# Kernel tuning notes

Measured on AMD Instinct MI355X. Metric: run time of the kernel, lower is better.

Reference implementation:

```python
import jax, jax.numpy as jnp
import numpy as np

N, NFEAT, NHID, NREL, NCLASS, NHEADS = 4096, 512, 64, 64, 16, 8
ALPHA = 0.2   # LeakyReLU negative slope
NEG = -9e15   # pyGAT mask value


def _gat_layer(x, rel, mask, adj_ad, W, a1, a2, concat):
    # x: [N, Fin], rel: [nrel, Fin], mask: [N, N] bool, adj_ad: [N, nrel]
    xr = x + adj_ad @ rel                 # relation-augmented node features
    h = xr @ W                            # [N, Fout]
    f1 = h @ a1                           # [N]  (a^T[Wh_i||Wh_j] = f1_i + f2_j)
    f2 = h @ a2                           # [N]
    e = jax.nn.leaky_relu(f1[:, None] + f2[None, :], ALPHA)  # [N, N]
    att = jax.nn.softmax(jnp.where(mask, e, NEG), axis=1)
    out = att @ h                         # [N, Fout]
    return jax.nn.elu(out) if concat else out


def setup_inputs() -> dict:
    key = jax.random.key(0)
    ks = jax.random.split(key, 12)
    x = jax.random.normal(ks[0], (N, NFEAT), jnp.float32)
    rel = jax.random.normal(ks[1], (NREL, NFEAT), jnp.float32)
    rel_dict = jax.random.randint(ks[2], (N,), 0, NREL, jnp.int32)
    adj = (jax.random.uniform(ks[3], (N, N)) < 0.01).astype(jnp.float32)
    adj = jnp.maximum(adj, jnp.eye(N, dtype=jnp.float32))  # self loops
    adj_ad = jax.random.uniform(ks[4], (N, NREL), jnp.float32)
    adj_ad = adj_ad / adj_ad.sum(axis=1, keepdims=True)
    s_in = 1.0 / np.sqrt(NFEAT)
    s_hid = 1.0 / np.sqrt(NHID)
    s_cat = 1.0 / np.sqrt(NHID * NHEADS)
    W_heads = jax.random.normal(ks[5], (NHEADS, NFEAT, NHID), jnp.float32) * s_in
    a1_heads = jax.random.normal(ks[6], (NHEADS, NHID), jnp.float32) * s_hid
    a2_heads = jax.random.normal(ks[7], (NHEADS, NHID), jnp.float32) * s_hid
    W_out = jax.random.normal(ks[8], (NHID * NHEADS, NFEAT), jnp.float32) * s_cat
    a1_out = jax.random.normal(ks[9], (NFEAT,), jnp.float32) * s_in
    a2_out = jax.random.normal(ks[10], (NFEAT,), jnp.float32) * s_in
    lin_W = jax.random.normal(ks[11], (NFEAT, NCLASS), jnp.float32) * s_in
    lin_b = jnp.zeros((NCLASS,), jnp.float32)
    return {"x": x, "rel": rel, "rel_dict": rel_dict, "adj": adj, "adj_ad": adj_ad,
            "W_heads": W_heads, "a1_heads": a1_heads, "a2_heads": a2_heads,
            "W_out": W_out, "a1_out": a1_out, "a2_out": a2_out,
            "lin_W": lin_W, "lin_b": lin_b}


def reference(x, rel, rel_dict, adj, adj_ad, W_heads, a1_heads, a2_heads,
              W_out, a1_out, a2_out, lin_W, lin_b):
    # dropout is identity at inference (training=False); rel_dict is only used
    # by the repo to build adj/adj_ad, so it is a non-math constant here.
    mask = adj > 0
    # multi-head GAT layer, heads fused via vmap then concatenated on feature dim
    heads = jax.vmap(lambda W, a1, a2: _gat_layer(x, rel, mask, adj_ad, W, a1, a2, True))(
        W_heads, a1_heads, a2_heads)                      # [H, N, NHID]
    hcat = jnp.moveaxis(heads, 0, 1).reshape(N, NHEADS * NHID)  # [N, H*NHID]
    h2 = _gat_layer(hcat, rel, mask, adj_ad, W_out, a1_out, a2_out, False)  # [N, NFEAT]
    logits = jax.nn.elu(h2 @ lin_W + lin_b)               # [N, NCLASS]
    return jax.nn.log_softmax(logits, axis=1)
```

## Files before the change

### kernel.cpp

```cpp
#include <hip/hip_runtime.h>

#define NN      4096
#define FEAT    512
#define KDIM    576
#define NHID    64
#define NHEADS  8
#define NCLS    16
#define MAXDEG  128
#define ALPHA   0.2f

typedef __bf16 bf16_t;
typedef __bf16 bf16x8_t __attribute__((ext_vector_type(8)));
typedef float  f32x4_t  __attribute__((ext_vector_type(4)));
typedef unsigned short us8_t __attribute__((ext_vector_type(8)));

__device__ inline unsigned short f2bf(float f) {
    unsigned int u = __float_as_uint(f);
    u += 0x7fffu + ((u >> 16) & 1u);
    return (unsigned short)(u >> 16);
}
__device__ inline float bfu2f(unsigned short b) {
    return __uint_as_float(((unsigned int)b) << 16);
}
__device__ inline void gload16(const void* g, void* s) {
    __builtin_amdgcn_global_load_lds(
        (const __attribute__((address_space(1))) void*)g,
        (__attribute__((address_space(3))) void*)s, 16, 0, 0);
}

#define PREP_REL0   0
#define PREP_TR0    256
#define PREP_Z0     384
#define PREP_CAST0  392
#define PREP_CSR0   2440
#define PREP_NBLK   3464

__global__ __launch_bounds__(256) void prep_kernel(
    const float* __restrict__ adj, int* __restrict__ deg, int* __restrict__ cols,
    const float* __restrict__ adj_ad, const float* __restrict__ rel,
    const float* __restrict__ x, bf16_t* __restrict__ Abf,
    bf16_t* __restrict__ Abf2,
    const float* __restrict__ Wh, const float* __restrict__ Wo,
    unsigned short* __restrict__ WcT, unsigned short* __restrict__ WoT,
    float* __restrict__ f1o, float* __restrict__ f2o) {
    int b = blockIdx.x;
    int t = threadIdx.x;
    __shared__ float smem[64 * 65];
    if (b < PREP_TR0) {
        int r  = b & 63;
        int nh = (b >> 6) & 1;
        int n  = nh * 256 + t;
        smem[t]       = rel[r * FEAT + t];
        smem[t + 256] = rel[r * FEAT + 256 + t];
        __syncthreads();
        float acc[8] = {};
        if (b < 128) {
            int h = n >> 6, f = n & 63;
            const float* p = Wh + (size_t)h * 32768 + f;
            for (int k0 = 0; k0 < 512; k0 += 8)
                #pragma unroll
                for (int u = 0; u < 8; ++u)
                    acc[u] += smem[k0 + u] * p[(size_t)(k0 + u) * 64];
            float s = ((acc[0] + acc[1]) + (acc[2] + acc[3]))
                    + ((acc[4] + acc[5]) + (acc[6] + acc[7]));
            WcT[(size_t)n * KDIM + 512 + r] = f2bf(s);
        } else {
            const float* p = Wo + n;
            for (int k0 = 0; k0 < 512; k0 += 8)
                #pragma unroll
                for (int u = 0; u < 8; ++u)
                    acc[u] += smem[k0 + u] * p[(size_t)(k0 + u) * 512];
            float s = ((acc[0] + acc[1]) + (acc[2] + acc[3]))
                    + ((acc[4] + acc[5]) + (acc[6] + acc[7]));
            WoT[(size_t)n * KDIM + 512 + r] = f2bf(s);
        }
    } else if (b < PREP_Z0) {
        int tb = b - PREP_TR0;
        if (tb < 64) {
            int h = tb >> 3, k0 = (tb & 7) * 64;
            const float* src = Wh + (size_t)h * 32768 + (size_t)k0 * 64;
            #pragma unroll
            for (int i2 = 0; i2 < 16; ++i2) {
                int li = t + i2 * 256;
                float v = src[li];
                smem[(li & 63) * 65 + (li >> 6)] = v;
            }
            __syncthreads();
            #pragma unroll
            for (int i2 = 0; i2 < 16; ++i2) {
                int li = t + i2 * 256;
                int f = li >> 6, r = li & 63;
                WcT[(size_t)(h * 64 + f) * KDIM + k0 + r] = f2bf(smem[f * 65 + r]);
            }
        } else {
            int wb = tb - 64;
            int n0 = (wb & 7) * 64, k0 = (wb >> 3) * 64;
            #pragma unroll
            for (int i2 = 0; i2 < 16; ++i2) {
                int li = t + i2 * 256;
                int r = li >> 6, f = li & 63;
                float v = Wo[(size_t)(k0 + r) * 512 + n0 + f];
                smem[f * 65 + r] = v;
            }
            __syncthreads();
            #pragma unroll
            for (int i2 = 0; i2 < 16; ++i2) {
                int li = t + i2 * 256;
                int f = li >> 6, r = li & 63;
                WoT[(size_t)(n0 + f) * KDIM + k0 + r] = f2bf(smem[f * 65 + r]);
            }
        }
    } else if (b < PREP_CAST0) {
        int g = (b - PREP_Z0) * 256 + t;
        if (g < 1024) ((float4*)f1o)[g] = make_float4(0.f, 0.f, 0.f, 0.f);
        else ((float4*)f2o)[g - 1024] = make_float4(0.f, 0.f, 0.f, 0.f);
    } else if (b < PREP_CSR0) {
        int half = t >> 7;
        int tt = t & 127;
        size_t i = (size_t)(b - PREP_CAST0) * 2 + half;
        float4 xv = ((const float4*)(x + i * FEAT))[tt];
        ushort4 o;
        o.x = f2bf(xv.x); o.y = f2bf(xv.y);
        o.z = f2bf(xv.z); o.w = f2bf(xv.w);
        *(ushort4*)(Abf + i * KDIM + 4 * tt) = o;
        if (tt < 16) {
            float4 av = ((const float4*)(adj_ad + i * 64))[tt];
            ushort4 o2;
            o2.x = f2bf(av.x); o2.y = f2bf(av.y);
            o2.z = f2bf(av.z); o2.w = f2bf(av.w);
            *(ushort4*)(Abf  + i * KDIM + 512 + 4 * tt) = o2;
            *(ushort4*)(Abf2 + i * KDIM + 512 + 4 * tt) = o2;
        }
    } else {
        int l = t & 63;
        int i = (b - PREP_CSR0) * 4 + (t >> 6);
        const float4* row4 = (const float4*)(adj + (size_t)i * NN);
        float4 v[16];
        #pragma unroll
        for (int c2 = 0; c2 < 16; ++c2) v[c2] = row4[l + c2 * 64];
        unsigned long long mask = 0;
        #pragma unroll
        for (int c2 = 0; c2 < 16; ++c2) {
            unsigned m4 = (unsigned)(v[c2].x > 0.0f)
                        | ((unsigned)(v[c2].y > 0.0f) << 1)
                        | ((unsigned)(v[c2].z > 0.0f) << 2)
                        | ((unsigned)(v[c2].w > 0.0f) << 3);
            mask |= (unsigned long long)m4 << (4 * c2);
        }
        int c = __popcll(mask);
        int pre = c;
        #pragma unroll
        for (int off = 1; off < 64; off <<= 1) {
            int n = __shfl_up(pre, off);
            if (l >= off) pre += n;
        }
        int base = pre - c;
        if (l == 63) deg[i] = pre > MAXDEG ? MAXDEG : pre;
        int* colrow = cols + i * MAXDEG;
        int idx = base;
        while (mask) {
            int bit = (int)__ffsll(mask) - 1;
            mask &= mask - 1;
            int j = 4 * l + ((bit >> 2) << 8) + (bit & 3);
            if (idx < MAXDEG) colrow[idx] = j;
            ++idx;
        }
    }
}

__global__ __launch_bounds__(256) void gemm_bf16_dot_kernel(
    const bf16_t* __restrict__ A, const bf16_t* __restrict__ Bt,
    unsigned short* __restrict__ Cbf,
    const float* __restrict__ a1, const float* __restrict__ a2,
    float* __restrict__ f1, float* __restrict__ f2, int layer2) {
    __shared__ __align__(16) bf16_t As[128][64];
    __shared__ __align__(16) bf16_t Bs[128][64];
    const int bm = blockIdx.x * 128;
    const int bn = blockIdx.y * 128;
    const int by = blockIdx.y;
    const int t  = threadIdx.x;
    const int l  = t & 63;
    const int w  = t >> 6;
    const int wr = w >> 1;
    const int wc = w & 1;
    const int c16 = l & 15;
    const int q8  = (l >> 4) * 8;
    const int r4  = (l >> 4) * 4;

    const bf16_t* Abase = A  + (size_t)bm * KDIM;
    const bf16_t* Bbase = Bt + (size_t)bn * KDIM;

    f32x4_t acc[4][4] = {};
    for (int k0 = 0; k0 < KDIM; k0 += 64) {
        #pragma unroll
        for (int c = 0; c < 4; ++c) {
            int cb = c * 256 + w * 64;
            int li = cb + l;
            gload16(Abase + (size_t)(li >> 3) * KDIM + k0 + (li & 7) * 8,
                    (char*)&As[0][0] + cb * 16);
        }
        #pragma unroll
        for (int c = 0; c < 4; ++c) {
            int cb = c * 256 + w * 64;
            int li = cb + l;
            gload16(Bbase + (size_t)(li >> 3) * KDIM + k0 + (li & 7) * 8,
                    (char*)&Bs[0][0] + cb * 16);
        }
        __syncthreads();
        #pragma unroll
        for (int kk = 0; kk < 64; kk += 32) {
            bf16x8_t af[4], bfr[4];
            #pragma unroll
            for (int mi = 0; mi < 4; ++mi)
                af[mi] = *(const bf16x8_t*)&As[wr * 64 + mi * 16 + c16][kk + q8];
            #pragma unroll
            for (int ni = 0; ni < 4; ++ni)
                bfr[ni] = *(const bf16x8_t*)&Bs[wc * 64 + ni * 16 + c16][kk + q8];
            #pragma unroll
            for (int mi = 0; mi < 4; ++mi)
                #pragma unroll
                for (int ni = 0; ni < 4; ++ni)
                    acc[mi][ni] = __builtin_amdgcn_mfma_f32_16x16x32_bf16(
                        af[mi], bfr[ni], acc[mi][ni], 0, 0, 0);
        }
        __syncthreads();
    }
    #pragma unroll
    for (int mi = 0; mi < 4; ++mi)
        #pragma unroll
        for (int ni = 0; ni < 4; ++ni)
            #pragma unroll
            for (int r = 0; r < 4; ++r)
                Cbf[(size_t)(bm + wr * 64 + mi * 16 + r4 + r) * FEAT
                    + bn + wc * 64 + ni * 16 + c16] = f2bf(acc[mi][ni][r]);

    float a1v[4], a2v[4];
    #pragma unroll
    for (int ni = 0; ni < 4; ++ni) {
        a1v[ni] = a1[bn + wc * 64 + ni * 16 + c16];
        a2v[ni] = a2[bn + wc * 64 + ni * 16 + c16];
    }
    float p1[4][4] = {}, p2[4][4] = {};
    #pragma unroll
    for (int mi = 0; mi < 4; ++mi)
        #pragma unroll
        for (int ni = 0; ni < 4; ++ni)
            #pragma unroll
            for (int r = 0; r < 4; ++r) {
                p1[mi][r] += acc[mi][ni][r] * a1v[ni];
                p2[mi][r] += acc[mi][ni][r] * a2v[ni];
            }
    #pragma unroll
    for (int off = 1; off <= 8; off <<= 1)
        #pragma unroll
        for (int mi = 0; mi < 4; ++mi)
            #pragma unroll
            for (int r = 0; r < 4; ++r) {
                p1[mi][r] += __shfl_xor(p1[mi][r], off);
                p2[mi][r] += __shfl_xor(p2[mi][r], off);
            }
    if (c16 == 0) {
        #pragma unroll
        for (int mi = 0; mi < 4; ++mi)
            #pragma unroll
            for (int r = 0; r < 4; ++r) {
                int row = bm + wr * 64 + mi * 16 + r4 + r;
                if (layer2) {
                    atomicAdd(&f1[row], p1[mi][r]);
                    atomicAdd(&f2[row], p2[mi][r]);
                } else {
                    f1[(by * 2 + wc) * NN + row] = p1[mi][r];
                    f2[(by * 2 + wc) * NN + row] = p2[mi][r];
                }
            }
    }
}

__global__ __launch_bounds__(512) void att1_kernel(
    const bf16_t* __restrict__ Hbf, const float* __restrict__ f1,
    const float* __restrict__ f2, const int* __restrict__ deg,
    const int* __restrict__ cols, bf16_t* __restrict__ outbf) {
    int i = blockIdx.x;
    int tid = threadIdx.x;
    int h = tid >> 6;
    int l = tid & 63;
    __shared__ int jl[MAXDEG];
    __shared__ float se[NHEADS][MAXDEG];
    __shared__ float part[NHEADS][FEAT];
    __shared__ float sinv[NHEADS];
    __shared__ int sdeg;
    if (tid == 0) sdeg = deg[i];
    __syncthreads();
    int d = sdeg;
    int dpad = (d + 63) & ~63;
    for (int k = tid; k < dpad; k += 512)
        jl[k] = (k < d) ? cols[i * MAXDEG + k] : i;
    __syncthreads();
    float fi = f1[h * NN + i];
    float lmax = -1e30f;
    for (int k = l; k < d; k += 64) {
        float e = fi + f2[h * NN + jl[k]];
        e = e > 0.0f ? e : ALPHA * e;
        se[h][k] = e;
        lmax = fmaxf(lmax, e);
    }
    for (int off = 32; off; off >>= 1) lmax = fmaxf(lmax, __shfl_down(lmax, off));
    float m = __shfl(lmax, 0);
    float ls = 0.0f;
    for (int k = l; k < d; k += 64) {
        float p = __expf(se[h][k] - m);
        se[h][k] = p;
        ls += p;
    }
    for (int k = d + l; k < dpad; k += 64) se[h][k] = 0.0f;
    for (int off = 32; off; off >>= 1) ls += __shfl_down(ls, off);
    if (l == 0) sinv[h] = 1.0f / ls;
    __syncthreads();
    const int myhead = l >> 3;
    float acc[8] = {};
    for (int k0 = 0; k0 < dpad; k0 += 64) {
        float pw[8];
        const bf16_t* rp[8];
        #pragma unroll
        for (int j = 0; j < 8; ++j) {
            int k = k0 + j * 8 + h;
            pw[j] = se[myhead][k];
            rp[j] = Hbf + (size_t)jl[k] * FEAT + l * 8;
        }
        #pragma unroll
        for (int j = 0; j < 8; ++j) {
            us8_t v = *(const us8_t*)rp[j];
            float p = pw[j];
            #pragma unroll
            for (int q = 0; q < 8; ++q) acc[q] += p * bfu2f(v[q]);
        }
    }
    *(float4*)&part[h][l * 8]     = make_float4(acc[0], acc[1], acc[2], acc[3]);
    *(float4*)&part[h][l * 8 + 4] = make_float4(acc[4], acc[5], acc[6], acc[7]);
    __syncthreads();
    {
        float sum = 0.0f;
        #pragma unroll
        for (int w2 = 0; w2 < NHEADS; ++w2) sum += part[w2][tid];
        float o = sum * sinv[tid >> 6];
        o = o > 0.0f ? o : __expf(o) - 1.0f;
        ((unsigned short*)outbf)[(size_t)i * KDIM + tid] = f2bf(o);
    }
}

__global__ __launch_bounds__(256) void att2_final_kernel(
    const bf16_t* __restrict__ Hbf, const float* __restrict__ f1,
    const float* __restrict__ f2, const int* __restrict__ deg,
    const int* __restrict__ cols, const float* __restrict__ linW,
    const float* __restrict__ linb, float* __restrict__ out) {
    int i = blockIdx.x;
    int t = threadIdx.x;
    __shared__ int jl[MAXDEG];
    __shared__ float sp[MAXDEG];
    __shared__ float red[4];
    __shared__ float part[3][FEAT];
    __shared__ float hrow[FEAT];
    __shared__ float clsred[16][NCLS];
    __shared__ float sl[NCLS];
    __shared__ int sdeg;
    if (t == 0) sdeg = deg[i];
    __syncthreads();
    int d = sdeg;
    int dpad = (d + 31) & ~31;
    if (t < dpad) jl[t] = (t < d) ? cols[i * MAXDEG + t] : i;
    __syncthreads();
    float e = 0.0f, lmax = -1e30f;
    if (t < d) {
        e = f1[i] + f2[jl[t]];
        e = e > 0.0f ? e : ALPHA * e;
        lmax = e;
    }
    for (int off = 32; off; off >>= 1) lmax = fmaxf(lmax, __shfl_down(lmax, off));
    if ((t & 63) == 0) red[t >> 6] = lmax;
    __syncthreads();
    float m = fmaxf(fmaxf(red[0], red[1]), fmaxf(red[2], red[3]));
    float p = 0.0f;
    if (t < d) p = __expf(e - m);
    if (t < dpad) sp[t] = p;
    float ls = p;
    for (int off = 32; off; off >>= 1) ls += __shfl_down(ls, off);
    __syncthreads();
    if ((t & 63) == 0) red[t >> 6] = ls;
    __syncthreads();
    float s = red[0] + red[1] + red[2] + red[3];
    float inv = 1.0f / s;
    const int slot = t >> 6;
    const int cg   = t & 63;
    float acc[8] = {};
    for (int k0 = 0; k0 < dpad; k0 += 32) {
        float pw[8];
        const bf16_t* rp[8];
        #pragma unroll
        for (int j = 0; j < 8; ++j) {
            int k = k0 + j * 4 + slot;
            pw[j] = sp[k];
            rp[j] = Hbf + (size_t)jl[k] * FEAT + cg * 8;
        }
        #pragma unroll
        for (int j = 0; j < 8; ++j) {
            us8_t v = *(const us8_t*)rp[j];
            float pk = pw[j];
            #pragma unroll
            for (int q = 0; q < 8; ++q) acc[q] += pk * bfu2f(v[q]);
        }
    }
    if (slot > 0) {
        float* dst = &part[slot - 1][cg * 8];
        *(float4*)(dst)     = make_float4(acc[0], acc[1], acc[2], acc[3]);
        *(float4*)(dst + 4) = make_float4(acc[4], acc[5], acc[6], acc[7]);
    }
    __syncthreads();
    if (slot == 0) {
        #pragma unroll
        for (int sl2 = 0; sl2 < 3; ++sl2)
            #pragma unroll
            for (int j = 0; j < 8; ++j) acc[j] += part[sl2][cg * 8 + j];
        float* dst = &hrow[cg * 8];
        *(float4*)(dst)     = make_float4(acc[0] * inv, acc[1] * inv, acc[2] * inv, acc[3] * inv);
        *(float4*)(dst + 4) = make_float4(acc[4] * inv, acc[5] * inv, acc[6] * inv, acc[7] * inv);
    }
    __syncthreads();
    {
        int c = t & 15;
        int seg = t >> 4;
        float partial = 0.0f;
        int f0 = seg * 32;
        #pragma unroll 8
        for (int f = f0; f < f0 + 32; ++f) partial += hrow[f] * linW[f * NCLS + c];
        clsred[seg][c] = partial;
    }
    __syncthreads();
    if (t < NCLS) {
        float logit = linb[t];
        #pragma unroll
        for (int seg = 0; seg < 16; ++seg) logit += clsred[seg][t];
        logit = logit > 0.0f ? logit : __expf(logit) - 1.0f;
        sl[t] = logit;
    }
    __syncthreads();
    if (t < NCLS) {
        float mm = sl[0];
        #pragma unroll
        for (int c = 1; c < NCLS; ++c) mm = fmaxf(mm, sl[c]);
        float ssum = 0.0f;
        #pragma unroll
        for (int c = 0; c < NCLS; ++c) ssum += __expf(sl[c] - mm);
        out[i * NCLS + t] = sl[t] - mm - logf(ssum);
    }
}

extern "C" void kernel_launch(void* const* d_in, const int* in_sizes, int n_in,
                              void* d_out, int out_size, void* d_ws, size_t ws_size,
                              hipStream_t stream) {
    const float* x        = (const float*)d_in[0];
    const float* rel      = (const float*)d_in[1];
    const float* adj      = (const float*)d_in[3];
    const float* adj_ad   = (const float*)d_in[4];
    const float* W_heads  = (const float*)d_in[5];
    const float* a1_heads = (const float*)d_in[6];
    const float* a2_heads = (const float*)d_in[7];
    const float* W_out    = (const float*)d_in[8];
    const float* a1_out   = (const float*)d_in[9];
    const float* a2_out   = (const float*)d_in[10];
    const float* lin_W    = (const float*)d_in[11];
    const float* lin_b    = (const float*)d_in[12];
    float* out = (float*)d_out;

    char* ws = (char*)d_ws;
    bf16_t* Abf  = (bf16_t*)(ws);
    bf16_t* Abf2 = (bf16_t*)(ws + (5u  << 20));
    bf16_t* Hbf1 = (bf16_t*)(ws + (10u << 20));
    bf16_t* Hbf2 = (bf16_t*)(ws + (14u << 20));
    bf16_t* WcT  = (bf16_t*)(ws + (18u << 20));
    bf16_t* WoT  = (bf16_t*)(ws + (19u << 20));
    float*  f1   = (float*) (ws + (20u << 20));
    float*  f2   = (float*) (ws + (20u << 20) + (128u << 10));
    float*  f1o  = (float*) (ws + (20u << 20) + (256u << 10));
    float*  f2o  = (float*) (ws + (20u << 20) + (272u << 10));
    int*    deg  = (int*)   (ws + (20u << 20) + (288u << 10));
    int*    cols = (int*)   (ws + (21u << 20));

    prep_kernel<<<PREP_NBLK, 256, 0, stream>>>(
        adj, deg, cols, adj_ad, rel, x, Abf, Abf2, W_heads, W_out,
        (unsigned short*)WcT, (unsigned short*)WoT, f1o, f2o);
    gemm_bf16_dot_kernel<<<dim3(32, 4), 256, 0, stream>>>(
        Abf, WcT, (unsigned short*)Hbf1, a1_heads, a2_heads, f1, f2, 0);
    att1_kernel<<<NN, 512, 0, stream>>>(Hbf1, f1, f2, deg, cols, Abf2);
    gemm_bf16_dot_kernel<<<dim3(32, 4), 256, 0, stream>>>(
        Abf2, WoT, (unsigned short*)Hbf2, a1_out, a2_out, f1o, f2o, 1);
    att2_final_kernel<<<NN, 256, 0, stream>>>(Hbf2, f1o, f2o, deg, cols, lin_W, lin_b, out);
}
```

Baseline: 207.4 us.

## Shrink GEMM tiles to 64x64 with XOR-swizzled LDS and trim attention padding

Halves the GEMM block tile from 128x128 to 64x64. This launches 512 workgroups instead of 128, so the grid can fill the GPU's compute units. An XOR swizzle is added to the LDS layout to avoid bank conflicts. Layer-1 f1/f2 partial dot products are now reduced per head with atomics into a zeroed buffer, and the prep kernel zeroes the whole contiguous f1/f2/f1o/f2o region. The attention kernels pad neighbor lists to smaller multiples, 32 and 16, to cut wasted gathers. In exchange, the smaller tiles reuse each loaded tile less and the change adds atomic traffic.

```diff
diff --git a/kernel.cpp b/kernel.cpp
--- a/kernel.cpp
+++ b/kernel.cpp
@@ -31,9 +31,9 @@
 #define PREP_REL0   0
 #define PREP_TR0    256
 #define PREP_Z0     384
-#define PREP_CAST0  392
-#define PREP_CSR0   2440
-#define PREP_NBLK   3464
+#define PREP_CAST0  456
+#define PREP_CSR0   2504
+#define PREP_NBLK   3528
 
 __global__ __launch_bounds__(256) void prep_kernel(
     const float* __restrict__ adj, int* __restrict__ deg, int* __restrict__ cols,
@@ -42,7 +42,7 @@
     bf16_t* __restrict__ Abf2,
     const float* __restrict__ Wh, const float* __restrict__ Wo,
     unsigned short* __restrict__ WcT, unsigned short* __restrict__ WoT,
-    float* __restrict__ f1o, float* __restrict__ f2o) {
+    float* __restrict__ fzero) {
     int b = blockIdx.x;
     int t = threadIdx.x;
     __shared__ float smem[64 * 65];
@@ -112,8 +112,7 @@
         }
     } else if (b < PREP_CAST0) {
         int g = (b - PREP_Z0) * 256 + t;
-        if (g < 1024) ((float4*)f1o)[g] = make_float4(0.f, 0.f, 0.f, 0.f);
-        else ((float4*)f2o)[g - 1024] = make_float4(0.f, 0.f, 0.f, 0.f);
+        ((float4*)fzero)[g] = make_float4(0.f, 0.f, 0.f, 0.f);
     } else if (b < PREP_CSR0) {
         int half = t >> 7;
         int tt = t & 127;
@@ -173,10 +172,10 @@
     unsigned short* __restrict__ Cbf,
     const float* __restrict__ a1, const float* __restrict__ a2,
     float* __restrict__ f1, float* __restrict__ f2, int layer2) {
-    __shared__ __align__(16) bf16_t As[128][64];
-    __shared__ __align__(16) bf16_t Bs[128][64];
-    const int bm = blockIdx.x * 128;
-    const int bn = blockIdx.y * 128;
+    __shared__ __align__(16) bf16_t As[64][64];
+    __shared__ __align__(16) bf16_t Bs[64][64];
+    const int bm = blockIdx.x * 64;
+    const int bn = blockIdx.y * 64;
     const int by = blockIdx.y;
     const int t  = threadIdx.x;
     const int l  = t & 63;
@@ -190,61 +189,70 @@
     const bf16_t* Abase = A  + (size_t)bm * KDIM;
     const bf16_t* Bbase = Bt + (size_t)bn * KDIM;
 
-    f32x4_t acc[4][4] = {};
+    f32x4_t acc[2][2] = {};
     for (int k0 = 0; k0 < KDIM; k0 += 64) {
         #pragma unroll
-        for (int c = 0; c < 4; ++c) {
+        for (int c = 0; c < 2; ++c) {
             int cb = c * 256 + w * 64;
             int li = cb + l;
-            gload16(Abase + (size_t)(li >> 3) * KDIM + k0 + (li & 7) * 8,
+            int r = li >> 3, pc = li & 7;
+            int lc = pc ^ (r & 7);
+            gload16(Abase + (size_t)r * KDIM + k0 + lc * 8,
                     (char*)&As[0][0] + cb * 16);
         }
         #pragma unroll
-        for (int c = 0; c < 4; ++c) {
+        for (int c = 0; c < 2; ++c) {
             int cb = c * 256 + w * 64;
             int li = cb + l;
-            gload16(Bbase + (size_t)(li >> 3) * KDIM + k0 + (li & 7) * 8,
+            int r = li >> 3, pc = li & 7;
+            int lc = pc ^ (r & 7);
+            gload16(Bbase + (size_t)r * KDIM + k0 + lc * 8,
                     (char*)&Bs[0][0] + cb * 16);
         }
         __syncthreads();
         #pragma unroll
         for (int kk = 0; kk < 64; kk += 32) {
-            bf16x8_t af[4], bfr[4];
-            #pragma unroll
-            for (int mi = 0; mi < 4; ++mi)
-                af[mi] = *(const bf16x8_t*)&As[wr * 64 + mi * 16 + c16][kk + q8];
-            #pragma unroll
-            for (int ni = 0; ni < 4; ++ni)
-                bfr[ni] = *(const bf16x8_t*)&Bs[wc * 64 + ni * 16 + c16][kk + q8];
-            #pragma unroll
-            for (int mi = 0; mi < 4; ++mi)
+            const int ck = (kk + q8) >> 3;
+            bf16x8_t af[2], bfr[2];
+            #pragma unroll
+            for (int mi = 0; mi < 2; ++mi) {
+                int R = wr * 32 + mi * 16 + c16;
+                af[mi] = *(const bf16x8_t*)&As[R][(ck ^ (R & 7)) * 8];
+            }
+            #pragma unroll
+            for (int ni = 0; ni < 2; ++ni) {
+                int R = wc * 32 + ni * 16 + c16;
+                bfr[ni] = *(const bf16x8_t*)&Bs[R][(ck ^ (R & 7)) * 8];
+            }
+            #pragma unroll
+            for (int mi = 0; mi < 2; ++mi)
                 #pragma unroll
-                for (int ni = 0; ni < 4; ++ni)
+                for (int ni = 0; ni < 2; ++ni)
                     acc[mi][ni] = __builtin_amdgcn_mfma_f32_16x16x32_bf16(
                         af[mi], bfr[ni], acc[mi][ni], 0, 0, 0);
         }
         __syncthreads();
     }
     #pragma unroll
-    for (int mi = 0; mi < 4; ++mi)
-        #pragma unroll
-        for (int ni = 0; ni < 4; ++ni)
+    for (int mi = 0; mi < 2; ++mi)
+        #pragma unroll
+        for (int ni = 0; ni < 2; ++ni)
             #pragma unroll
             for (int r = 0; r < 4; ++r)
-                Cbf[(size_t)(bm + wr * 64 + mi * 16 + r4 + r) * FEAT
-                    + bn + wc * 64 + ni * 16 + c16] = f2bf(acc[mi][ni][r]);
-
-    float a1v[4], a2v[4];
+                Cbf[(size_t)(bm + wr * 32 + mi * 16 + r4 + r) * FEAT
+                    + bn + wc * 32 + ni * 16 + c16] = f2bf(acc[mi][ni][r]);
+
+    float a1v[2], a2v[2];
     #pragma unroll
-    for (int ni = 0; ni < 4; ++ni) {
-        a1v[ni] = a1[bn + wc * 64 + ni * 16 + c16];
-        a2v[ni] = a2[bn + wc * 64 + ni * 16 + c16];
-    }
-    float p1[4][4] = {}, p2[4][4] = {};
+    for (int ni = 0; ni < 2; ++ni) {
+        a1v[ni] = a1[bn + wc * 32 + ni * 16 + c16];
+        a2v[ni] = a2[bn + wc * 32 + ni * 16 + c16];
+    }
+    float p1[2][4] = {}, p2[2][4] = {};
     #pragma unroll
-    for (int mi = 0; mi < 4; ++mi)
-        #pragma unroll
-        for (int ni = 0; ni < 4; ++ni)
+    for (int mi = 0; mi < 2; ++mi)
+        #pragma unroll
+        for (int ni = 0; ni < 2; ++ni)
             #pragma unroll
             for (int r = 0; r < 4; ++r) {
                 p1[mi][r] += acc[mi][ni][r] * a1v[ni];
@@ -253,25 +261,21 @@
     #pragma unroll
     for (int off = 1; off <= 8; off <<= 1)
         #pragma unroll
-        for (int mi = 0; mi < 4; ++mi)
+        for (int mi = 0; mi < 2; ++mi)
             #pragma unroll
             for (int r = 0; r < 4; ++r) {
                 p1[mi][r] += __shfl_xor(p1[mi][r], off);
                 p2[mi][r] += __shfl_xor(p2[mi][r], off);
             }
     if (c16 == 0) {
-        #pragma unroll
-        for (int mi = 0; mi < 4; ++mi)
+        int fbase = layer2 ? 0 : by * NN;
+        #pragma unroll
+        for (int mi = 0; mi < 2; ++mi)
             #pragma unroll
             for (int r = 0; r < 4; ++r) {
-                int row = bm + wr * 64 + mi * 16 + r4 + r;
-                if (layer2) {
-                    atomicAdd(&f1[row], p1[mi][r]);
-                    atomicAdd(&f2[row], p2[mi][r]);
-                } else {
-                    f1[(by * 2 + wc) * NN + row] = p1[mi][r];
-                    f2[(by * 2 + wc) * NN + row] = p2[mi][r];
-                }
+                int row = bm + wr * 32 + mi * 16 + r4 + r;
+                atomicAdd(&f1[fbase + row], p1[mi][r]);
+                atomicAdd(&f2[fbase + row], p2[mi][r]);
             }
     }
 }
@@ -292,7 +296,7 @@
     if (tid == 0) sdeg = deg[i];
     __syncthreads();
     int d = sdeg;
-    int dpad = (d + 63) & ~63;
+    int dpad = (d + 31) & ~31;
     for (int k = tid; k < dpad; k += 512)
         jl[k] = (k < d) ? cols[i * MAXDEG + k] : i;
     __syncthreads();
@@ -318,17 +322,17 @@
     __syncthreads();
     const int myhead = l >> 3;
     float acc[8] = {};
-    for (int k0 = 0; k0 < dpad; k0 += 64) {
-        float pw[8];
-        const bf16_t* rp[8];
-        #pragma unroll
-        for (int j = 0; j < 8; ++j) {
+    for (int k0 = 0; k0 < dpad; k0 += 32) {
+        float pw[4];
+        const bf16_t* rp[4];
+        #pragma unroll
+        for (int j = 0; j < 4; ++j) {
             int k = k0 + j * 8 + h;
             pw[j] = se[myhead][k];
             rp[j] = Hbf + (size_t)jl[k] * FEAT + l * 8;
         }
         #pragma unroll
-        for (int j = 0; j < 8; ++j) {
+        for (int j = 0; j < 4; ++j) {
             us8_t v = *(const us8_t*)rp[j];
             float p = pw[j];
             #pragma unroll
@@ -366,7 +370,7 @@
     if (t == 0) sdeg = deg[i];
     __syncthreads();
     int d = sdeg;
-    int dpad = (d + 31) & ~31;
+    int dpad = (d + 15) & ~15;
     if (t < dpad) jl[t] = (t < d) ? cols[i * MAXDEG + t] : i;
     __syncthreads();
     float e = 0.0f, lmax = -1e30f;
@@ -392,17 +396,17 @@
     const int slot = t >> 6;
     const int cg   = t & 63;
     float acc[8] = {};
-    for (int k0 = 0; k0 < dpad; k0 += 32) {
-        float pw[8];
-        const bf16_t* rp[8];
-        #pragma unroll
-        for (int j = 0; j < 8; ++j) {
+    for (int k0 = 0; k0 < dpad; k0 += 16) {
+        float pw[4];
+        const bf16_t* rp[4];
+        #pragma unroll
+        for (int j = 0; j < 4; ++j) {
             int k = k0 + j * 4 + slot;
             pw[j] = sp[k];
             rp[j] = Hbf + (size_t)jl[k] * FEAT + cg * 8;
         }
         #pragma unroll
-        for (int j = 0; j < 8; ++j) {
+        for (int j = 0; j < 4; ++j) {
             us8_t v = *(const us8_t*)rp[j];
             float pk = pw[j];
             #pragma unroll
@@ -487,11 +491,11 @@
 
     prep_kernel<<<PREP_NBLK, 256, 0, stream>>>(
         adj, deg, cols, adj_ad, rel, x, Abf, Abf2, W_heads, W_out,
-        (unsigned short*)WcT, (unsigned short*)WoT, f1o, f2o);
-    gemm_bf16_dot_kernel<<<dim3(32, 4), 256, 0, stream>>>(
+        (unsigned short*)WcT, (unsigned short*)WoT, f1);
+    gemm_bf16_dot_kernel<<<dim3(64, 8), 256, 0, stream>>>(
         Abf, WcT, (unsigned short*)Hbf1, a1_heads, a2_heads, f1, f2, 0);
     att1_kernel<<<NN, 512, 0, stream>>>(Hbf1, f1, f2, deg, cols, Abf2);
-    gemm_bf16_dot_kernel<<<dim3(32, 4), 256, 0, stream>>>(
+    gemm_bf16_dot_kernel<<<dim3(64, 8), 256, 0, stream>>>(
         Abf2, WoT, (unsigned short*)Hbf2, a1_out, a2_out, f1o, f2o, 1);
     att2_final_kernel<<<NN, 256, 0, stream>>>(Hbf2, f1o, f2o, deg, cols, lin_W, lin_b, out);
 }
```

Result: faster. 189.7 us (-8.5%).
